# Optimization experiments

Measured on AMD Instinct MI355X. Metric: run time of the kernel, lower is better.

## Reference

```python
import jax, jax.numpy as jnp
import numpy as np

B, S, D = 2, 2048, 768
E, L = 4, 2
H = 4 * D  # dim_mlp = dim * mlp_ratio
EPS = 1e-6


def setup_inputs() -> dict:
    key = jax.random.key(0)
    ks = jax.random.split(key, 4)
    x = jax.random.normal(ks[0], (B, S, D), dtype=jnp.float32)
    expert_idx = jax.random.randint(ks[1], (B, S), 0, E, dtype=jnp.int32)
    # Linear weights: normal(std=0.02), biases zero (per init_weights).
    W1 = 0.02 * jax.random.normal(ks[2], (L, E, D, H), dtype=jnp.float32)
    b1 = jnp.zeros((L, E, H), dtype=jnp.float32)
    W2 = 0.02 * jax.random.normal(ks[3], (L, E, H, D), dtype=jnp.float32)
    b2 = jnp.zeros((L, E, D), dtype=jnp.float32)
    # LayerNorm: weight=1, bias=0 (per init_weights).
    ln_g = jnp.ones((L, D), dtype=jnp.float32)
    ln_b = jnp.zeros((L, D), dtype=jnp.float32)
    return {"x": x, "expert_idx": expert_idx, "W1": W1, "b1": b1,
            "W2": W2, "b2": b2, "ln_g": ln_g, "ln_b": ln_b}


def _layernorm(x, g, b):
    mu = jnp.mean(x, axis=-1, keepdims=True)
    var = jnp.mean(jnp.square(x - mu), axis=-1, keepdims=True)
    return (x - mu) * jax.lax.rsqrt(var + EPS) * g + b


def reference(x, expert_idx, W1, b1, W2, b2, ln_g, ln_b):
    # Eval mode: Dropout and DropPath are identity.
    idx = expert_idx[:, :, None, None]  # [B,S,1,1] for gather over expert axis
    for i in range(L):
        h = _layernorm(x, ln_g[i], ln_b[i])                       # [B,S,D]
        # All experts' FFNs computed densely (as in the torch module).
        a = jnp.einsum('bsd,edh->bseh', h, W1[i]) + b1[i]         # [B,S,E,H]
        a = jax.nn.gelu(a, approximate=False)                     # exact GELU (nn.GELU)
        y = jnp.einsum('bseh,ehd->bsed', a, W2[i]) + b2[i]        # [B,S,E,D] == feat_all
        # Per-token gather of the selected expert's slice.
        sel = jnp.take_along_axis(y, idx, axis=2)[:, :, 0, :]     # [B,S,D]
        x = x + sel
    return x
```

## Files before the change

kernel.cpp:

```cpp
#include <hip/hip_runtime.h>
#include <hip/hip_bf16.h>

#define T_TOK 4096
#define DD 768
#define HH 3072
#define EE 4
#define LL 2
#define NELT (T_TOK * DD)

typedef __attribute__((ext_vector_type(8))) short short8;
typedef __attribute__((ext_vector_type(4))) float f32x4;

__device__ __forceinline__ float bf2f(ushort u) { return __uint_as_float(((unsigned)u) << 16); }
__device__ __forceinline__ ushort f2bf(float f) {
  unsigned x = __float_as_uint(f);
  return (ushort)((x + 0x7fffu + ((x >> 16) & 1u)) >> 16);
}

__device__ __forceinline__ void gl2lds16(const void* g, void* l) {
  __builtin_amdgcn_global_load_lds((const __attribute__((address_space(1))) void*)g,
                                   (__attribute__((address_space(3))) void*)l, 16, 0, 0);
}

__global__ __launch_bounds__(256) void prep_kernel(const int* __restrict__ eidx,
                                                   int* __restrict__ inv,
                                                   int* __restrict__ meta) {
  __shared__ int cnt[EE], cur[EE], offs[EE];
  int t = threadIdx.x;
  if (t < EE) { cnt[t] = 0; cur[t] = 0; }
  __syncthreads();
  for (int i = t; i < T_TOK; i += 256) atomicAdd(&cnt[eidx[i]], 1);
  __syncthreads();
  if (t == 0) {
    int off = 0, nt = 0;
    for (int e = 0; e < EE; e++) {
      meta[e] = off; offs[e] = off;
      int c = cnt[e];
      int n = (c + 63) >> 6;
      for (int k = 0; k < n; k++) { meta[8 + nt] = e; meta[96 + nt] = k << 6; nt++; }
      off += c;
    }
    meta[4] = off;
    meta[5] = nt;
  }
  __syncthreads();
  for (int i = t; i < T_TOK; i += 256) {
    int e = eidx[i];
    inv[i] = offs[e] + atomicAdd(&cur[e], 1);
  }
}

template <bool HASY, bool WRITEX>
__global__ __launch_bounds__(256) void ln_kernel(const float* __restrict__ x,
                                                 const float* __restrict__ y,
                                                 const float* __restrict__ g,
                                                 const float* __restrict__ b,
                                                 const int* __restrict__ inv,
                                                 ushort* __restrict__ h,
                                                 float* __restrict__ xf) {
  int wid = blockIdx.x * 4 + (threadIdx.x >> 6);
  int lane = threadIdx.x & 63;
  int pos = inv[wid];
  const float* xr = x + (size_t)wid * DD;
  const float* y0 = y + (size_t)pos * DD;
  const float* y1 = y0 + NELT;
  float v[12], s = 0.f, ss = 0.f;
#pragma unroll
  for (int i = 0; i < 12; i++) {
    int c = lane + i * 64;
    float vv = xr[c];
    if (HASY) vv += y0[c] + y1[c];
    if (WRITEX) xf[(size_t)wid * DD + c] = vv;
    v[i] = vv;
    s += vv; ss += vv * vv;
  }
#pragma unroll
  for (int o = 32; o; o >>= 1) { s += __shfl_xor(s, o, 64); ss += __shfl_xor(ss, o, 64); }
  float mu = s * (1.f / DD);
  float var = ss * (1.f / DD) - mu * mu;
  float rs = rsqrtf(var + 1e-6f);
  ushort* hr = h + (size_t)pos * DD;
#pragma unroll
  for (int i = 0; i < 12; i++) {
    int c = lane + i * 64;
    hr[c] = f2bf((v[i] - mu) * rs * g[c] + b[c]);
  }
}

__global__ __launch_bounds__(256) void store_kernel(const float* __restrict__ xf,
                                                    const float* __restrict__ y,
                                                    const int* __restrict__ inv,
                                                    float* __restrict__ out) {
  int wid = blockIdx.x * 4 + (threadIdx.x >> 6);
  int lane = threadIdx.x & 63;
  int pos = inv[wid];
  const float* xr = xf + (size_t)wid * DD;
  const float* y0 = y + (size_t)pos * DD;
  const float* y1 = y0 + NELT;
  float* o = out + (size_t)wid * DD;
#pragma unroll
  for (int i = 0; i < 12; i++) {
    int c = lane + i * 64;
    o[c] = xr[c] + y0[c] + y1[c];
  }
}

__global__ __launch_bounds__(256) void transpose_f32_bf16(const float* __restrict__ src,
                                                          ushort* __restrict__ dst,
                                                          int R, int C) {
  __shared__ ushort tile[64][68];
  size_t mo = (size_t)blockIdx.z * R * C;
  src += mo;
  dst += mo;
  int c0 = blockIdx.x * 64, r0 = blockIdx.y * 64;
  int t = threadIdx.x;
  int tr = t >> 4;
  int tc = (t & 15) << 2;
#pragma unroll
  for (int i = 0; i < 4; i++) {
    int r = tr + i * 16;
    float4 v = *(const float4*)(src + (size_t)(r0 + r) * C + (c0 + tc));
    tile[r][tc] = f2bf(v.x); tile[r][tc + 1] = f2bf(v.y);
    tile[r][tc + 2] = f2bf(v.z); tile[r][tc + 3] = f2bf(v.w);
  }
  __syncthreads();
#pragma unroll
  for (int i = 0; i < 4; i++) {
    int c = tr + i * 16;
    ushort4 v;
    v.x = tile[tc][c]; v.y = tile[tc + 1][c]; v.z = tile[tc + 2][c]; v.w = tile[tc + 3][c];
    *(ushort4*)(dst + (size_t)(c0 + c) * R + (r0 + tc)) = v;
  }
}

template <int KTOT, int KLEN, int NTOT, bool GELU>
__global__ __launch_bounds__(256, 4) void gemm_kernel(const ushort* __restrict__ A,
                                                      const ushort* __restrict__ Bt,
                                                      const float* __restrict__ bias,
                                                      void* __restrict__ Cout,
                                                      const int* __restrict__ meta) {
  int ty = blockIdx.y;
  if (ty >= meta[5]) return;
  int e = meta[8 + ty];
  int mstart = meta[96 + ty];
  int off0 = meta[e];
  int cnt = meta[e + 1] - off0;
  int ntile = blockIdx.x;
  int z = blockIdx.z;
  int kbegin = z * KLEN;

  __shared__ __align__(16) ushort lds[12288];
  ushort* As = lds;
  ushort* Bs = lds + 4096;

  int tid = threadIdx.x;
  int w = tid >> 6, lane = tid & 63;

  int rr = lane >> 3;
  int swz = ((lane & 7) ^ rr) * 8;
  const ushort* agp[2];
  const ushort* bgp[4];
  ushort* alp[2];
  ushort* blp[4];
#pragma unroll
  for (int i = 0; i < 2; i++) {
    int r = w * 16 + i * 8;
    int arow = off0 + min(mstart + r + rr, cnt - 1);
    agp[i] = A + (size_t)arow * KTOT + kbegin + swz;
    alp[i] = As + r * 64 + lane * 8;
  }
#pragma unroll
  for (int i = 0; i < 4; i++) {
    int r = w * 32 + i * 8;
    int brow = e * NTOT + ntile * 128 + r + rr;
    bgp[i] = Bt + (size_t)brow * KTOT + kbegin + swz;
    blp[i] = Bs + r * 64 + lane * 8;
  }

  int wm = (w >> 1) * 32, wn = (w & 1) * 64;
  int qm = lane & 15;
  int quad = lane >> 4;
  int s7 = qm & 7;

  f32x4 acc[2][4];
#pragma unroll
  for (int mi = 0; mi < 2; mi++)
#pragma unroll
    for (int ni = 0; ni < 4; ni++) acc[mi][ni] = (f32x4){0.f, 0.f, 0.f, 0.f};

  for (int k0 = 0; k0 < KLEN; k0 += 64) {
#pragma unroll
    for (int i = 0; i < 2; i++) gl2lds16(agp[i] + k0, alp[i]);
#pragma unroll
    for (int i = 0; i < 4; i++) gl2lds16(bgp[i] + k0, blp[i]);
    __syncthreads();
#pragma unroll
    for (int h2 = 0; h2 < 2; h2++) {
      int lchunk = ((h2 * 4 + quad) ^ s7) * 8;
      short8 af[2], bfr[4];
#pragma unroll
      for (int mi = 0; mi < 2; mi++)
        af[mi] = *(const short8*)(As + (wm + mi * 16 + qm) * 64 + lchunk);
#pragma unroll
      for (int ni = 0; ni < 4; ni++)
        bfr[ni] = *(const short8*)(Bs + (wn + ni * 16 + qm) * 64 + lchunk);
#pragma unroll
      for (int mi = 0; mi < 2; mi++)
#pragma unroll
        for (int ni = 0; ni < 4; ni++)
          acc[mi][ni] = __builtin_amdgcn_mfma_f32_16x16x32_bf16(af[mi], bfr[ni], acc[mi][ni], 0, 0, 0);
    }
    __syncthreads();
  }

  int rbase = quad * 4;
  float bv[4];
#pragma unroll
  for (int ni = 0; ni < 4; ni++)
    bv[ni] = (!GELU && z != 0) ? 0.f : bias[e * NTOT + ntile * 128 + wn + ni * 16 + qm];

  if (GELU) {
#pragma unroll
    for (int mi = 0; mi < 2; mi++)
#pragma unroll
      for (int ni = 0; ni < 4; ni++) {
        int c = wn + ni * 16 + qm;
#pragma unroll
        for (int r = 0; r < 4; r++) {
          float vv = acc[mi][ni][r] + bv[ni];
          vv = 0.5f * vv * (1.f + erff(vv * 0.70710678118f));
          lds[(wm + mi * 16 + rbase + r) * 128 + c] = f2bf(vv);
        }
      }
    __syncthreads();
    int row0 = tid >> 4;
    int cseg = (tid & 15) * 8;
    ushort* aout = (ushort*)Cout;
#pragma unroll
    for (int it = 0; it < 4; it++) {
      int row = it * 16 + row0;
      int mg = mstart + row;
      if (mg < cnt) {
        short8 v = *(const short8*)(lds + row * 128 + cseg);
        *(short8*)(aout + (size_t)(off0 + mg) * HH + ntile * 128 + cseg) = v;
      }
    }
  } else {
    float* y = (float*)Cout + (size_t)z * NELT;
#pragma unroll
    for (int mi = 0; mi < 2; mi++) {
#pragma unroll
      for (int r = 0; r < 4; r++) {
        int mg = mstart + wm + mi * 16 + rbase + r;
        if (mg >= cnt) continue;
        float* crow = y + (size_t)(off0 + mg) * DD + ntile * 128;
#pragma unroll
        for (int ni = 0; ni < 4; ni++)
          crow[wn + ni * 16 + qm] = acc[mi][ni][r] + bv[ni];
      }
    }
  }
}

extern "C" void kernel_launch(void* const* d_in, const int* in_sizes, int n_in,
                              void* d_out, int out_size, void* d_ws, size_t ws_size,
                              hipStream_t stream) {
  const float* x   = (const float*)d_in[0];
  const int*  eidx = (const int*)d_in[1];
  const float* W1  = (const float*)d_in[2];
  const float* b1  = (const float*)d_in[3];
  const float* W2  = (const float*)d_in[4];
  const float* b2  = (const float*)d_in[5];
  const float* lng = (const float*)d_in[6];
  const float* lnb = (const float*)d_in[7];

  char* ws = (char*)d_ws;
  float*  xf   = (float*)(ws + 0);
  ushort* h    = (ushort*)(ws + 12582912);
  ushort* a    = (ushort*)(ws + 18874368);
  ushort* Wt   = (ushort*)(ws + 44040192);
  float*  y    = (float*)(ws + 62914560);
  int*    inv  = (int*)(ws + 88080384);
  int*    meta = (int*)(ws + 88096768);

  prep_kernel<<<1, 256, 0, stream>>>(eidx, inv, meta);

  for (int l = 0; l < LL; l++) {
    if (l == 0)
      ln_kernel<false, false><<<T_TOK / 4, 256, 0, stream>>>(
          x, y, lng, lnb, inv, h, xf);
    else
      ln_kernel<true, true><<<T_TOK / 4, 256, 0, stream>>>(
          x, y, lng + l * DD, lnb + l * DD, inv, h, xf);
    transpose_f32_bf16<<<dim3(HH / 64, DD / 64, EE), 256, 0, stream>>>(
        W1 + (size_t)l * EE * DD * HH, Wt, DD, HH);
    gemm_kernel<DD, DD, HH, true><<<dim3(HH / 128, 68), 256, 0, stream>>>(
        h, Wt, b1 + l * EE * HH, (void*)a, meta);
    transpose_f32_bf16<<<dim3(DD / 64, HH / 64, EE), 256, 0, stream>>>(
        W2 + (size_t)l * EE * HH * DD, Wt, HH, DD);
    gemm_kernel<HH, HH / 2, DD, false><<<dim3(DD / 128, 68, 2), 256, 0, stream>>>(
        a, Wt, b2 + l * EE * DD, (void*)y, meta);
  }

  store_kernel<<<T_TOK / 4, 256, 0, stream>>>(xf, y, inv, (float*)d_out);
}
```

Before: 392.4 us.

## Use 128x128 GEMM tiles, 4-way split-K, and bf16 partial outputs

Grows the per-block M tile from 64 to 128 rows, so each warp computes a 64x64 sub-tile and B operand reuse doubles; expert tile scheduling is changed to 128-row chunks. The second GEMM now splits K four ways instead of two, and its partial results are stored as bf16 through a shared LDS-staged vectorized epilogue rather than scattered fp32 stores. The LN and store kernels sum four bf16 partials. This cuts global traffic and raises arithmetic intensity, but it adds padding waste for experts whose token counts are not multiples of 128, uses more registers and LDS, and loses precision in the bf16 partial sums.

```diff
diff --git a/kernel.cpp b/kernel.cpp
--- a/kernel.cpp
+++ b/kernel.cpp
@@ -7,6 +7,7 @@
 #define EE 4
 #define LL 2
 #define NELT (T_TOK * DD)
+#define NSPLIT 4
 
 typedef __attribute__((ext_vector_type(8))) short short8;
 typedef __attribute__((ext_vector_type(4))) float f32x4;
@@ -36,8 +37,8 @@
     for (int e = 0; e < EE; e++) {
       meta[e] = off; offs[e] = off;
       int c = cnt[e];
-      int n = (c + 63) >> 6;
-      for (int k = 0; k < n; k++) { meta[8 + nt] = e; meta[96 + nt] = k << 6; nt++; }
+      int n = (c + 127) >> 7;
+      for (int k = 0; k < n; k++) { meta[8 + nt] = e; meta[96 + nt] = k << 7; nt++; }
       off += c;
     }
     meta[4] = off;
@@ -52,7 +53,7 @@
 
 template <bool HASY, bool WRITEX>
 __global__ __launch_bounds__(256) void ln_kernel(const float* __restrict__ x,
-                                                 const float* __restrict__ y,
+                                                 const ushort* __restrict__ y,
                                                  const float* __restrict__ g,
                                                  const float* __restrict__ b,
                                                  const int* __restrict__ inv,
@@ -62,14 +63,16 @@
   int lane = threadIdx.x & 63;
   int pos = inv[wid];
   const float* xr = x + (size_t)wid * DD;
-  const float* y0 = y + (size_t)pos * DD;
-  const float* y1 = y0 + NELT;
+  const ushort* yp = y + (size_t)pos * DD;
   float v[12], s = 0.f, ss = 0.f;
 #pragma unroll
   for (int i = 0; i < 12; i++) {
     int c = lane + i * 64;
     float vv = xr[c];
-    if (HASY) vv += y0[c] + y1[c];
+    if (HASY) {
+#pragma unroll
+      for (int z = 0; z < NSPLIT; z++) vv += bf2f(yp[c + (size_t)z * NELT]);
+    }
     if (WRITEX) xf[(size_t)wid * DD + c] = vv;
     v[i] = vv;
     s += vv; ss += vv * vv;
@@ -88,20 +91,22 @@
 }
 
 __global__ __launch_bounds__(256) void store_kernel(const float* __restrict__ xf,
-                                                    const float* __restrict__ y,
+                                                    const ushort* __restrict__ y,
                                                     const int* __restrict__ inv,
                                                     float* __restrict__ out) {
   int wid = blockIdx.x * 4 + (threadIdx.x >> 6);
   int lane = threadIdx.x & 63;
   int pos = inv[wid];
   const float* xr = xf + (size_t)wid * DD;
-  const float* y0 = y + (size_t)pos * DD;
-  const float* y1 = y0 + NELT;
+  const ushort* yp = y + (size_t)pos * DD;
   float* o = out + (size_t)wid * DD;
 #pragma unroll
   for (int i = 0; i < 12; i++) {
     int c = lane + i * 64;
-    o[c] = xr[c] + y0[c] + y1[c];
+    float vv = xr[c];
+#pragma unroll
+    for (int z = 0; z < NSPLIT; z++) vv += bf2f(yp[c + (size_t)z * NELT]);
+    o[c] = vv;
   }
 }
 
@@ -137,7 +142,7 @@
 __global__ __launch_bounds__(256, 4) void gemm_kernel(const ushort* __restrict__ A,
                                                       const ushort* __restrict__ Bt,
                                                       const float* __restrict__ bias,
-                                                      void* __restrict__ Cout,
+                                                      ushort* __restrict__ Cout,
                                                       const int* __restrict__ meta) {
   int ty = blockIdx.y;
   if (ty >= meta[5]) return;
@@ -149,63 +154,60 @@
   int z = blockIdx.z;
   int kbegin = z * KLEN;
 
-  __shared__ __align__(16) ushort lds[12288];
+  __shared__ __align__(16) ushort lds[16384];
   ushort* As = lds;
-  ushort* Bs = lds + 4096;
+  ushort* Bs = lds + 8192;
 
   int tid = threadIdx.x;
   int w = tid >> 6, lane = tid & 63;
 
   int rr = lane >> 3;
   int swz = ((lane & 7) ^ rr) * 8;
-  const ushort* agp[2];
+  const ushort* agp[4];
   const ushort* bgp[4];
-  ushort* alp[2];
+  ushort* alp[4];
   ushort* blp[4];
 #pragma unroll
-  for (int i = 0; i < 2; i++) {
-    int r = w * 16 + i * 8;
+  for (int i = 0; i < 4; i++) {
+    int r = w * 32 + i * 8;
     int arow = off0 + min(mstart + r + rr, cnt - 1);
     agp[i] = A + (size_t)arow * KTOT + kbegin + swz;
     alp[i] = As + r * 64 + lane * 8;
-  }
-#pragma unroll
-  for (int i = 0; i < 4; i++) {
-    int r = w * 32 + i * 8;
     int brow = e * NTOT + ntile * 128 + r + rr;
     bgp[i] = Bt + (size_t)brow * KTOT + kbegin + swz;
     blp[i] = Bs + r * 64 + lane * 8;
   }
 
-  int wm = (w >> 1) * 32, wn = (w & 1) * 64;
+  int wm = (w >> 1) * 64, wn = (w & 1) * 64;
   int qm = lane & 15;
   int quad = lane >> 4;
   int s7 = qm & 7;
 
-  f32x4 acc[2][4];
-#pragma unroll
-  for (int mi = 0; mi < 2; mi++)
+  f32x4 acc[4][4];
+#pragma unroll
+  for (int mi = 0; mi < 4; mi++)
 #pragma unroll
     for (int ni = 0; ni < 4; ni++) acc[mi][ni] = (f32x4){0.f, 0.f, 0.f, 0.f};
 
   for (int k0 = 0; k0 < KLEN; k0 += 64) {
 #pragma unroll
-    for (int i = 0; i < 2; i++) gl2lds16(agp[i] + k0, alp[i]);
-#pragma unroll
-    for (int i = 0; i < 4; i++) gl2lds16(bgp[i] + k0, blp[i]);
+    for (int i = 0; i < 4; i++) {
+      gl2lds16(agp[i] + k0, alp[i]);
+      gl2lds16(bgp[i] + k0, blp[i]);
+    }
     __syncthreads();
 #pragma unroll
     for (int h2 = 0; h2 < 2; h2++) {
       int lchunk = ((h2 * 4 + quad) ^ s7) * 8;
-      short8 af[2], bfr[4];
-#pragma unroll
-      for (int mi = 0; mi < 2; mi++)
+      short8 af[4], bfr[4];
+#pragma unroll
+      for (int mi = 0; mi < 4; mi++)
         af[mi] = *(const short8*)(As + (wm + mi * 16 + qm) * 64 + lchunk);
 #pragma unroll
       for (int ni = 0; ni < 4; ni++)
         bfr[ni] = *(const short8*)(Bs + (wn + ni * 16 + qm) * 64 + lchunk);
 #pragma unroll
-      for (int mi = 0; mi < 2; mi++)
+      for (int mi = 0; mi < 4; mi++)
 #pragma unroll
         for (int ni = 0; ni < 4; ni++)
           acc[mi][ni] = __builtin_amdgcn_mfma_f32_16x16x32_bf16(af[mi], bfr[ni], acc[mi][ni], 0, 0, 0);
@@ -219,45 +221,31 @@
   for (int ni = 0; ni < 4; ni++)
     bv[ni] = (!GELU && z != 0) ? 0.f : bias[e * NTOT + ntile * 128 + wn + ni * 16 + qm];
 
-  if (GELU) {
-#pragma unroll
-    for (int mi = 0; mi < 2; mi++)
-#pragma unroll
-      for (int ni = 0; ni < 4; ni++) {
-        int c = wn + ni * 16 + qm;
-#pragma unroll
-        for (int r = 0; r < 4; r++) {
-          float vv = acc[mi][ni][r] + bv[ni];
-          vv = 0.5f * vv * (1.f + erff(vv * 0.70710678118f));
-          lds[(wm + mi * 16 + rbase + r) * 128 + c] = f2bf(vv);
-        }
+#pragma unroll
+  for (int mi = 0; mi < 4; mi++)
+#pragma unroll
+    for (int ni = 0; ni < 4; ni++) {
+      int c = wn + ni * 16 + qm;
+#pragma unroll
+      for (int r = 0; r < 4; r++) {
+        float vv = acc[mi][ni][r] + bv[ni];
+        if (GELU) vv = 0.5f * vv * (1.f + erff(vv * 0.70710678118f));
+        lds[(wm + mi * 16 + rbase + r) * 128 + c] = f2bf(vv);
       }
-    __syncthreads();
-    int row0 = tid >> 4;
-    int cseg = (tid & 15) * 8;
-    ushort* aout = (ushort*)Cout;
-#pragma unroll
-    for (int it = 0; it < 4; it++) {
-      int row = it * 16 + row0;
-      int mg = mstart + row;
-      if (mg < cnt) {
-        short8 v = *(const short8*)(lds + row * 128 + cseg);
-        *(short8*)(aout + (size_t)(off0 + mg) * HH + ntile * 128 + cseg) = v;
-      }
-    }
-  } else {
-    float* y = (float*)Cout + (size_t)z * NELT;
-#pragma unroll
-    for (int mi = 0; mi < 2; mi++) {
-#pragma unroll
-      for (int r = 0; r < 4; r++) {
-        int mg = mstart + wm + mi * 16 + rbase + r;
-        if (mg >= cnt) continue;
-        float* crow = y + (size_t)(off0 + mg) * DD + ntile * 128;
-#pragma unroll
-        for (int ni = 0; ni < 4; ni++)
-          crow[wn + ni * 16 + qm] = acc[mi][ni][r] + bv[ni];
-      }
+    }
+  __syncthreads();
+  int row0 = tid >> 4;
+  int cseg = (tid & 15) * 8;
+#pragma unroll
+  for (int it = 0; it < 8; it++) {
+    int row = it * 16 + row0;
+    int mg = mstart + row;
+    if (mg < cnt) {
+      short8 v = *(const short8*)(lds + row * 128 + cseg);
+      if (GELU)
+        *(short8*)(Cout + (size_t)(off0 + mg) * HH + ntile * 128 + cseg) = v;
+      else
+        *(short8*)(Cout + (size_t)z * NELT + (size_t)(off0 + mg) * DD + ntile * 128 + cseg) = v;
     }
   }
 }
@@ -279,7 +267,7 @@
   ushort* h    = (ushort*)(ws + 12582912);
   ushort* a    = (ushort*)(ws + 18874368);
   ushort* Wt   = (ushort*)(ws + 44040192);
-  float*  y    = (float*)(ws + 62914560);
+  ushort* y    = (ushort*)(ws + 62914560);
   int*    inv  = (int*)(ws + 88080384);
   int*    meta = (int*)(ws + 88096768);
 
@@ -294,12 +282,12 @@
           x, y, lng + l * DD, lnb + l * DD, inv, h, xf);
     transpose_f32_bf16<<<dim3(HH / 64, DD / 64, EE), 256, 0, stream>>>(
         W1 + (size_t)l * EE * DD * HH, Wt, DD, HH);
-    gemm_kernel<DD, DD, HH, true><<<dim3(HH / 128, 68), 256, 0, stream>>>(
-        h, Wt, b1 + l * EE * HH, (void*)a, meta);
+    gemm_kernel<DD, DD, HH, true><<<dim3(HH / 128, 36), 256, 0, stream>>>(
+        h, Wt, b1 + l * EE * HH, a, meta);
     transpose_f32_bf16<<<dim3(DD / 64, HH / 64, EE), 256, 0, stream>>>(
         W2 + (size_t)l * EE * HH * DD, Wt, HH, DD);
-    gemm_kernel<HH, HH / 2, DD, false><<<dim3(DD / 128, 68, 2), 256, 0, stream>>>(
-        a, Wt, b2 + l * EE * DD, (void*)y, meta);
+    gemm_kernel<HH, HH / NSPLIT, DD, false><<<dim3(DD / 128, 36, NSPLIT), 256, 0, stream>>>(
+        a, Wt, b2 + l * EE * DD, y, meta);
   }
 
   store_kernel<<<T_TOK / 4, 256, 0, stream>>>(xf, y, inv, (float*)d_out);
```

Result: slower. 489.5 us (+24.7%).

## Batch weight transposes into fewer launches and widen GEMM1 N-tile to 256

Applied to the files above, without the earlier changes.

Weight transposes for W1 and W2 are merged into one kernel, and when workspace allows, all layers are converted in a single up-front launch rather than interleaved per layer. This cuts launch count and lets transposes run with more parallelism. The first GEMM now uses a 128x... 64x256 tile (NI=8) with lower occupancy target, raising A-tile reuse per B load. The workspace layout is rearranged, and the bigger tile raises register pressure and halves the block count for GEMM1.

```diff
diff --git a/kernel.cpp b/kernel.cpp
--- a/kernel.cpp
+++ b/kernel.cpp
@@ -105,14 +105,18 @@
   }
 }
 
-__global__ __launch_bounds__(256) void transpose_f32_bf16(const float* __restrict__ src,
-                                                          ushort* __restrict__ dst,
-                                                          int R, int C) {
+__global__ __launch_bounds__(256) void transpose_pair(const float* __restrict__ W1,
+                                                      const float* __restrict__ W2,
+                                                      ushort* __restrict__ dst_base,
+                                                      int zoff) {
   __shared__ ushort tile[64][68];
-  size_t mo = (size_t)blockIdx.z * R * C;
-  src += mo;
-  dst += mo;
-  int c0 = blockIdx.x * 64, r0 = blockIdx.y * 64;
+  int zs = blockIdx.z + zoff;
+  int e = zs & 3, which = (zs >> 2) & 1, l = zs >> 3;
+  const float* src = (which ? W2 : W1) + ((size_t)l * EE + e) * ((size_t)DD * HH);
+  ushort* dst = dst_base + (size_t)blockIdx.z * ((size_t)DD * HH);
+  int R, C, r0, c0;
+  if (which) { R = HH; C = DD; r0 = blockIdx.x * 64; c0 = blockIdx.y * 64; }
+  else       { R = DD; C = HH; r0 = blockIdx.y * 64; c0 = blockIdx.x * 64; }
   int t = threadIdx.x;
   int tr = t >> 4;
   int tc = (t & 15) << 2;
@@ -133,12 +137,14 @@
   }
 }
 
-template <int KTOT, int KLEN, int NTOT, bool GELU>
-__global__ __launch_bounds__(256, 4) void gemm_kernel(const ushort* __restrict__ A,
-                                                      const ushort* __restrict__ Bt,
-                                                      const float* __restrict__ bias,
-                                                      void* __restrict__ Cout,
-                                                      const int* __restrict__ meta) {
+template <int KTOT, int KLEN, int NTOT, int BN, bool GELU>
+__global__ __launch_bounds__(256, BN == 256 ? 3 : 4)
+void gemm_kernel(const ushort* __restrict__ A,
+                 const ushort* __restrict__ Bt,
+                 const float* __restrict__ bias,
+                 void* __restrict__ Cout,
+                 const int* __restrict__ meta) {
+  constexpr int NI = BN / 32;
   int ty = blockIdx.y;
   if (ty >= meta[5]) return;
   int e = meta[8 + ty];
@@ -149,9 +155,9 @@
   int z = blockIdx.z;
   int kbegin = z * KLEN;
 
-  __shared__ __align__(16) ushort lds[12288];
+  __shared__ __align__(16) ushort lds[(64 + BN) * 64];
   ushort* As = lds;
-  ushort* Bs = lds + 4096;
+  ushort* Bs = lds + 64 * 64;
 
   int tid = threadIdx.x;
   int w = tid >> 6, lane = tid & 63;
@@ -159,9 +165,7 @@
   int rr = lane >> 3;
   int swz = ((lane & 7) ^ rr) * 8;
   const ushort* agp[2];
-  const ushort* bgp[4];
   ushort* alp[2];
-  ushort* blp[4];
 #pragma unroll
   for (int i = 0; i < 2; i++) {
     int r = w * 16 + i * 8;
@@ -169,80 +173,84 @@
     agp[i] = A + (size_t)arow * KTOT + kbegin + swz;
     alp[i] = As + r * 64 + lane * 8;
   }
-#pragma unroll
-  for (int i = 0; i < 4; i++) {
-    int r = w * 32 + i * 8;
-    int brow = e * NTOT + ntile * 128 + r + rr;
+  const ushort* bgp[NI];
+  ushort* blp[NI];
+#pragma unroll
+  for (int i = 0; i < NI; i++) {
+    int r = w * (BN / 4) + i * 8;
+    int brow = e * NTOT + ntile * BN + r + rr;
     bgp[i] = Bt + (size_t)brow * KTOT + kbegin + swz;
     blp[i] = Bs + r * 64 + lane * 8;
   }
 
-  int wm = (w >> 1) * 32, wn = (w & 1) * 64;
+  int wm = (w >> 1) * 32, wn = (w & 1) * (BN / 2);
   int qm = lane & 15;
   int quad = lane >> 4;
   int s7 = qm & 7;
 
-  f32x4 acc[2][4];
+  f32x4 acc[2][NI];
 #pragma unroll
   for (int mi = 0; mi < 2; mi++)
 #pragma unroll
-    for (int ni = 0; ni < 4; ni++) acc[mi][ni] = (f32x4){0.f, 0.f, 0.f, 0.f};
+    for (int ni = 0; ni < NI; ni++) acc[mi][ni] = (f32x4){0.f, 0.f, 0.f, 0.f};
 
   for (int k0 = 0; k0 < KLEN; k0 += 64) {
 #pragma unroll
     for (int i = 0; i < 2; i++) gl2lds16(agp[i] + k0, alp[i]);
 #pragma unroll
-    for (int i = 0; i < 4; i++) gl2lds16(bgp[i] + k0, blp[i]);
+    for (int i = 0; i < NI; i++) gl2lds16(bgp[i] + k0, blp[i]);
     __syncthreads();
 #pragma unroll
     for (int h2 = 0; h2 < 2; h2++) {
       int lchunk = ((h2 * 4 + quad) ^ s7) * 8;
-      short8 af[2], bfr[4];
+      short8 af[2], bfr[NI];
 #pragma unroll
       for (int mi = 0; mi < 2; mi++)
         af[mi] = *(const short8*)(As + (wm + mi * 16 + qm) * 64 + lchunk);
 #pragma unroll
-      for (int ni = 0; ni < 4; ni++)
+      for (int ni = 0; ni < NI; ni++)
         bfr[ni] = *(const short8*)(Bs + (wn + ni * 16 + qm) * 64 + lchunk);
 #pragma unroll
       for (int mi = 0; mi < 2; mi++)
 #pragma unroll
-        for (int ni = 0; ni < 4; ni++)
+        for (int ni = 0; ni < NI; ni++)
           acc[mi][ni] = __builtin_amdgcn_mfma_f32_16x16x32_bf16(af[mi], bfr[ni], acc[mi][ni], 0, 0, 0);
     }
     __syncthreads();
   }
 
   int rbase = quad * 4;
-  float bv[4];
-#pragma unroll
-  for (int ni = 0; ni < 4; ni++)
-    bv[ni] = (!GELU && z != 0) ? 0.f : bias[e * NTOT + ntile * 128 + wn + ni * 16 + qm];
+  float bv[NI];
+#pragma unroll
+  for (int ni = 0; ni < NI; ni++)
+    bv[ni] = (!GELU && z != 0) ? 0.f : bias[e * NTOT + ntile * BN + wn + ni * 16 + qm];
 
   if (GELU) {
 #pragma unroll
     for (int mi = 0; mi < 2; mi++)
 #pragma unroll
-      for (int ni = 0; ni < 4; ni++) {
+      for (int ni = 0; ni < NI; ni++) {
         int c = wn + ni * 16 + qm;
 #pragma unroll
         for (int r = 0; r < 4; r++) {
           float vv = acc[mi][ni][r] + bv[ni];
           vv = 0.5f * vv * (1.f + erff(vv * 0.70710678118f));
-          lds[(wm + mi * 16 + rbase + r) * 128 + c] = f2bf(vv);
+          lds[(wm + mi * 16 + rbase + r) * BN + c] = f2bf(vv);
         }
       }
     __syncthreads();
-    int row0 = tid >> 4;
-    int cseg = (tid & 15) * 8;
+    constexpr int CH = BN / 8;
+    constexpr int RP = 256 / CH;
+    int row0 = tid / CH;
+    int cseg = (tid % CH) * 8;
     ushort* aout = (ushort*)Cout;
 #pragma unroll
-    for (int it = 0; it < 4; it++) {
-      int row = it * 16 + row0;
+    for (int it = 0; it < 64 / RP; it++) {
+      int row = it * RP + row0;
       int mg = mstart + row;
       if (mg < cnt) {
-        short8 v = *(const short8*)(lds + row * 128 + cseg);
-        *(short8*)(aout + (size_t)(off0 + mg) * HH + ntile * 128 + cseg) = v;
+        short8 v = *(const short8*)(lds + row * BN + cseg);
+        *(short8*)(aout + (size_t)(off0 + mg) * NTOT + ntile * BN + cseg) = v;
       }
     }
   } else {
@@ -253,9 +261,9 @@
       for (int r = 0; r < 4; r++) {
         int mg = mstart + wm + mi * 16 + rbase + r;
         if (mg >= cnt) continue;
-        float* crow = y + (size_t)(off0 + mg) * DD + ntile * 128;
-#pragma unroll
-        for (int ni = 0; ni < 4; ni++)
+        float* crow = y + (size_t)(off0 + mg) * DD + ntile * BN;
+#pragma unroll
+        for (int ni = 0; ni < NI; ni++)
           crow[wn + ni * 16 + qm] = acc[mi][ni][r] + bv[ni];
       }
     }
@@ -278,28 +286,41 @@
   float*  xf   = (float*)(ws + 0);
   ushort* h    = (ushort*)(ws + 12582912);
   ushort* a    = (ushort*)(ws + 18874368);
-  ushort* Wt   = (ushort*)(ws + 44040192);
-  float*  y    = (float*)(ws + 62914560);
-  int*    inv  = (int*)(ws + 88080384);
-  int*    meta = (int*)(ws + 88096768);
+  float*  y    = (float*)(ws + 44040192);
+  int*    inv  = (int*)(ws + 69206016);
+  int*    meta = (int*)(ws + 69222400);
+  ushort* Wt   = (ushort*)(ws + 69238784);
+  const size_t WSLOT = (size_t)EE * DD * HH;
+
+  int tier = (ws_size >= 69238784 + 8 * WSLOT * sizeof(ushort)) ? 2
+           : (ws_size >= 69238784 + 4 * WSLOT * sizeof(ushort)) ? 1 : 0;
 
   prep_kernel<<<1, 256, 0, stream>>>(eidx, inv, meta);
+  if (tier == 2)
+    transpose_pair<<<dim3(48, 12, 16), 256, 0, stream>>>(W1, W2, Wt, 0);
 
   for (int l = 0; l < LL; l++) {
     if (l == 0)
-      ln_kernel<false, false><<<T_TOK / 4, 256, 0, stream>>>(
-          x, y, lng, lnb, inv, h, xf);
+      ln_kernel<false, false><<<T_TOK / 4, 256, 0, stream>>>(x, y, lng, lnb, inv, h, xf);
     else
-      ln_kernel<true, true><<<T_TOK / 4, 256, 0, stream>>>(
-          x, y, lng + l * DD, lnb + l * DD, inv, h, xf);
-    transpose_f32_bf16<<<dim3(HH / 64, DD / 64, EE), 256, 0, stream>>>(
-        W1 + (size_t)l * EE * DD * HH, Wt, DD, HH);
-    gemm_kernel<DD, DD, HH, true><<<dim3(HH / 128, 68), 256, 0, stream>>>(
-        h, Wt, b1 + l * EE * HH, (void*)a, meta);
-    transpose_f32_bf16<<<dim3(DD / 64, HH / 64, EE), 256, 0, stream>>>(
-        W2 + (size_t)l * EE * HH * DD, Wt, HH, DD);
-    gemm_kernel<HH, HH / 2, DD, false><<<dim3(DD / 128, 68, 2), 256, 0, stream>>>(
-        a, Wt, b2 + l * EE * DD, (void*)y, meta);
+      ln_kernel<true, true><<<T_TOK / 4, 256, 0, stream>>>(x, y, lng + l * DD, lnb + l * DD, inv, h, xf);
+
+    if (tier == 1)
+      transpose_pair<<<dim3(48, 12, 8), 256, 0, stream>>>(W1, W2, Wt, l * 8);
+    else if (tier == 0)
+      transpose_pair<<<dim3(48, 12, 4), 256, 0, stream>>>(W1, W2, Wt, l * 8);
+
+    const ushort* Bt1 = (tier == 2) ? Wt + (size_t)(2 * l) * WSLOT : Wt;
+    gemm_kernel<DD, DD, HH, 256, true><<<dim3(HH / 256, 68), 256, 0, stream>>>(
+        h, Bt1, b1 + l * EE * HH, (void*)a, meta);
+
+    if (tier == 0)
+      transpose_pair<<<dim3(48, 12, 4), 256, 0, stream>>>(W1, W2, Wt, l * 8 + 4);
+
+    const ushort* Bt2 = (tier == 2) ? Wt + (size_t)(2 * l + 1) * WSLOT
+                       : (tier == 1) ? Wt + WSLOT : Wt;
+    gemm_kernel<HH, HH / 2, DD, 128, false><<<dim3(DD / 128, 68, 2), 256, 0, stream>>>(
+        a, Bt2, b2 + l * EE * DD, (void*)y, meta);
   }
 
   store_kernel<<<T_TOK / 4, 256, 0, stream>>>(xf, y, inv, (float*)d_out);
```

After: 414.9 us. 5.7% more time.
